# Kernel optimization log

Measured on AMD Instinct MI355X. Metric: run time of the kernel, lower is better.

## Reference

```python
import jax, jax.numpy as jnp
import numpy as np

N_HEAD = 16
HEAD_DIM = 64
ROPE_BASE = 10000.0


def _rope_tables(seq_len, head_dim):
    inv_freq = 1.0 / (ROPE_BASE ** (jnp.arange(0, head_dim, 2, dtype=jnp.float32) / head_dim))
    freqs = jnp.arange(seq_len, dtype=jnp.float32)[:, None] * inv_freq[None, :]  # (T, D/2)
    return jnp.cos(freqs), jnp.sin(freqs)


def _apply_rope(x, cos, sin):
    # x: (B, H, T, D); cos/sin: (T, D/2) broadcast to (1,1,T,D/2)
    x_even = x[..., ::2]
    x_odd = x[..., 1::2]
    re = x_even * cos - x_odd * sin
    ro = x_even * sin + x_odd * cos
    return jnp.stack((re, ro), axis=-1).reshape(x.shape)


def setup_inputs() -> dict:
    key = jax.random.key(0)
    ks = jax.random.split(key, 5)
    B, T, C = 4, 2048, 1024
    return {
        "x": jax.random.normal(ks[0], (B, T, C), dtype=jnp.float32),
        "qkv_w": jax.random.normal(ks[1], (3 * C, C), dtype=jnp.float32) * 0.02,
        "qkv_b": jax.random.normal(ks[2], (3 * C,), dtype=jnp.float32) * 0.02,
        "out_w": jax.random.normal(ks[3], (C, C), dtype=jnp.float32) * 0.02,
        "out_b": jax.random.normal(ks[4], (C,), dtype=jnp.float32) * 0.02,
    }


def reference(x, qkv_w, qkv_b, out_w, out_b):
    B, T, C = x.shape
    H, D = N_HEAD, HEAD_DIM
    qkv = x @ qkv_w.T + qkv_b                       # (B, T, 3C)
    qkv = qkv.reshape(B, T, 3, H, D).transpose(2, 0, 3, 1, 4)  # (3, B, H, T, D)
    q, k, v = qkv[0], qkv[1], qkv[2]
    cos, sin = _rope_tables(T, D)
    cos = cos[None, None]
    sin = sin[None, None]
    q = _apply_rope(q, cos, sin)
    k = _apply_rope(k, cos, sin)
    scores = jnp.einsum('bhtd,bhsd->bhts', q, k) / jnp.sqrt(jnp.float32(D))
    causal = jnp.tril(jnp.ones((T, T), dtype=bool))
    scores = jnp.where(causal[None, None], scores, -jnp.inf)
    weights = jax.nn.softmax(scores, axis=-1)
    out = jnp.einsum('bhts,bhsd->bhtd', weights, v)  # (B, H, T, D)
    out = out.transpose(0, 2, 1, 3).reshape(B, T, C)
    return out @ out_w.T + out_b
```

## Files before the change

kernel.cpp:

```cpp
#include <hip/hip_runtime.h>

#define B_ 4
#define T_ 2048
#define C_ 1024
#define H_ 16
#define D_ 64
#define M_ (B_*T_)
#define N1_ (3*C_)

typedef __bf16 bf16;
typedef __bf16 bf16x8 __attribute__((ext_vector_type(8)));
typedef __bf16 bf16x4 __attribute__((ext_vector_type(4)));
typedef float f32x4 __attribute__((ext_vector_type(4)));

#define GLOAD_LDS16(g, l) \
    __builtin_amdgcn_global_load_lds((const __attribute__((address_space(1))) void*)(g), \
                                     (__attribute__((address_space(3))) void*)(l), 16, 0, 0)

__global__ void k_conv3(const float* __restrict__ x, const float* __restrict__ w1,
                        const float* __restrict__ w2, bf16* __restrict__ xb,
                        bf16* __restrict__ wb1, bf16* __restrict__ wb2) {
    long i = ((long)blockIdx.x * 256 + threadIdx.x) * 4;
    const float* src; bf16* dst; long off;
    if (i < 8388608L)       { src = x;  dst = xb;  off = i; }
    else if (i < 11534336L) { src = w1; dst = wb1; off = i - 8388608L; }
    else                    { src = w2; dst = wb2; off = i - 11534336L; }
    float4 v = *(const float4*)(src + off);
    bf16x4 o; o[0] = (bf16)v.x; o[1] = (bf16)v.y; o[2] = (bf16)v.z; o[3] = (bf16)v.w;
    *(bf16x4*)(dst + off) = o;
}

__global__ __launch_bounds__(256) void k_gemm_qkv(const bf16* __restrict__ A,
                                                  const bf16* __restrict__ W,
                                                  const float* __restrict__ bias,
                                                  bf16* __restrict__ qr,
                                                  bf16* __restrict__ kr,
                                                  bf16* __restrict__ vt) {
    __shared__ __align__(16) bf16 As[128 * 32];
    __shared__ __align__(16) bf16 Ws[128 * 32];
    const int tid = threadIdx.x;
    const int lane16 = tid & 15;
    const int quad = (tid & 63) >> 4;
    const int wave = tid >> 6;
    const int wm = (wave >> 1) * 64, wn = (wave & 1) * 64;
    const long m0 = (long)blockIdx.y * 128;
    const long n0 = (long)blockIdx.x * 128;
    const int K = C_;

    f32x4 acc[4][4] = {};

    const int ra = tid >> 2, sa = tid & 3;
    const bf16* Ab0 = A + (m0 + ra) * K + sa * 8;
    const bf16* Ab1 = Ab0 + 64 * K;
    const bf16* Wb0 = W + (n0 + ra) * K + sa * 8;
    const bf16* Wb1 = Wb0 + 64 * K;
    bf16* Ad0 = As + tid * 8;
    bf16* Ad1 = As + tid * 8 + 2048;
    bf16* Wd0 = Ws + tid * 8;
    bf16* Wd1 = Ws + tid * 8 + 2048;

    for (int kt = 0; kt < K; kt += 32) {
        __syncthreads();
        GLOAD_LDS16(Ab0 + kt, Ad0);
        GLOAD_LDS16(Ab1 + kt, Ad1);
        GLOAD_LDS16(Wb0 + kt, Wd0);
        GLOAD_LDS16(Wb1 + kt, Wd1);
        __syncthreads();
        bf16x8 af[4], wf[4];
#pragma unroll
        for (int i = 0; i < 4; i++)
            af[i] = *(const bf16x8*)(As + (wm + i * 16 + lane16) * 32 + quad * 8);
#pragma unroll
        for (int i = 0; i < 4; i++)
            wf[i] = *(const bf16x8*)(Ws + (wn + i * 16 + lane16) * 32 + quad * 8);
#pragma unroll
        for (int mi = 0; mi < 4; mi++)
#pragma unroll
            for (int ni = 0; ni < 4; ni++)
                acc[mi][ni] = __builtin_amdgcn_mfma_f32_16x16x32_bf16(
                    af[mi], wf[ni], acc[mi][ni], 0, 0, 0);
    }

    const int sect = (int)blockIdx.x >> 3;
    const int bloc = (int)(m0 >> 11);
    const int tloc0 = ((int)m0 & 2047) + wm + quad * 4;

    if (sect < 2) {
        bf16* dst = (sect == 0) ? qr : kr;
#pragma unroll
        for (int ni = 0; ni < 4; ni++) {
            int n = (int)n0 + wn + ni * 16 + lane16;
            int d = n & 63;
            int h = (n >> 6) & 15;
            float bn = bias[n];
            float inv = exp2f(-0.415241011861f * (float)(d >> 1));
            float sb, cb; sincosf((float)tloc0 * inv, &sb, &cb);
            float s1, c1; sincosf(inv, &s1, &c1);
            float s16, c16; sincosf(16.0f * inv, &s16, &c16);
            bf16* base = dst + ((long)(bloc * 16 + h) * T_) * 64 + d;
#pragma unroll
            for (int mi = 0; mi < 4; mi++) {
                float cm = cb, sm = sb;
#pragma unroll
                for (int r = 0; r < 4; r++) {
                    float v = acc[mi][ni][r] + bn;
                    float vp = __shfl_xor(v, 1, 64);
                    float outv = (d & 1) ? (vp * sm + v * cm) : (v * cm - vp * sm);
                    base[(long)(tloc0 + mi * 16 + r) * 64] = (bf16)outv;
                    float cm2 = cm * c1 - sm * s1;
                    float sm2 = sm * c1 + cm * s1;
                    cm = cm2; sm = sm2;
                }
                float cb2 = cb * c16 - sb * s16;
                float sb2 = sb * c16 + cb * s16;
                cb = cb2; sb = sb2;
            }
        }
    } else {
#pragma unroll
        for (int ni = 0; ni < 4; ni++) {
            int n = (int)n0 + wn + ni * 16 + lane16;
            int d = n & 63;
            int h = (n >> 6) & 15;
            float bn = bias[n];
            bf16* base = vt + ((long)(bloc * 16 + h) * 64 + d) * T_ + tloc0;
#pragma unroll
            for (int mi = 0; mi < 4; mi++) {
                bf16x4 w;
#pragma unroll
                for (int r = 0; r < 4; r++) w[r] = (bf16)(acc[mi][ni][r] + bn);
                *(bf16x4*)(base + mi * 16) = w;
            }
        }
    }
}

__global__ __launch_bounds__(256) void k_gemm_out(const bf16* __restrict__ A,
                                                  const bf16* __restrict__ W,
                                                  const float* __restrict__ bias,
                                                  float* __restrict__ Cout) {
    __shared__ __align__(16) bf16 As[128 * 32];
    __shared__ __align__(16) bf16 Ws[128 * 32];
    const int tid = threadIdx.x;
    const int lane16 = tid & 15;
    const int quad = (tid & 63) >> 4;
    const int wave = tid >> 6;
    const int wm = (wave >> 1) * 64, wn = (wave & 1) * 64;
    const long m0 = (long)blockIdx.y * 128;
    const long n0 = (long)blockIdx.x * 128;
    const int K = C_, N = C_;

    f32x4 acc[4][4] = {};

    const int ra = tid >> 2, sa = tid & 3;
    const bf16* Ab0 = A + (m0 + ra) * K + sa * 8;
    const bf16* Ab1 = Ab0 + 64 * K;
    const bf16* Wb0 = W + (n0 + ra) * K + sa * 8;
    const bf16* Wb1 = Wb0 + 64 * K;
    bf16* Ad0 = As + tid * 8;
    bf16* Ad1 = As + tid * 8 + 2048;
    bf16* Wd0 = Ws + tid * 8;
    bf16* Wd1 = Ws + tid * 8 + 2048;

    for (int kt = 0; kt < K; kt += 32) {
        __syncthreads();
        GLOAD_LDS16(Ab0 + kt, Ad0);
        GLOAD_LDS16(Ab1 + kt, Ad1);
        GLOAD_LDS16(Wb0 + kt, Wd0);
        GLOAD_LDS16(Wb1 + kt, Wd1);
        __syncthreads();
        bf16x8 af[4], wf[4];
#pragma unroll
        for (int i = 0; i < 4; i++)
            af[i] = *(const bf16x8*)(As + (wm + i * 16 + lane16) * 32 + quad * 8);
#pragma unroll
        for (int i = 0; i < 4; i++)
            wf[i] = *(const bf16x8*)(Ws + (wn + i * 16 + lane16) * 32 + quad * 8);
#pragma unroll
        for (int mi = 0; mi < 4; mi++)
#pragma unroll
            for (int ni = 0; ni < 4; ni++)
                acc[mi][ni] = __builtin_amdgcn_mfma_f32_16x16x32_bf16(
                    af[mi], wf[ni], acc[mi][ni], 0, 0, 0);
    }

#pragma unroll
    for (int ni = 0; ni < 4; ni++) {
        long n = n0 + wn + ni * 16 + lane16;
        float bn = bias[n];
#pragma unroll
        for (int mi = 0; mi < 4; mi++) {
            long m = m0 + wm + mi * 16 + quad * 4;
#pragma unroll
            for (int r = 0; r < 4; r++)
                Cout[(m + r) * N + n] = acc[mi][ni][r] + bn;
        }
    }
}

__global__ __launch_bounds__(256) void k_flash(const bf16* __restrict__ qr,
                                               const bf16* __restrict__ kr,
                                               const bf16* __restrict__ vt,
                                               bf16* __restrict__ attn) {
    __shared__ __align__(16) bf16 Ks[64 * 72];
    __shared__ __align__(16) bf16 Vs[64 * 72];
    __shared__ __align__(16) bf16 Pl[8 * 16 * 72];

    const int bh = blockIdx.y;
    const int b = bh >> 4, h = bh & 15;
    const int tid = threadIdx.x;
    const int lane16 = tid & 15, quad = (tid & 63) >> 4;
    const int wave = tid >> 6;
    const int srow = tid >> 3, sch = tid & 7;

    const bf16* kbase = kr + (long)bh * T_ * 64;
    const bf16* vbase = vt + (long)bh * 64 * T_;
    bf16* Pw[2] = { Pl + (wave * 2 + 0) * (16 * 72), Pl + (wave * 2 + 1) * (16 * 72) };

    bf16x8 k0 = *(const bf16x8*)(kbase + (long)srow * 64 + sch * 8);
    bf16x8 k1 = *(const bf16x8*)(kbase + (long)(srow + 32) * 64 + sch * 8);
    bf16x8 v0 = *(const bf16x8*)(vbase + (long)srow * T_ + sch * 8);
    bf16x8 v1 = *(const bf16x8*)(vbase + (long)(srow + 32) * T_ + sch * 8);

    for (int phase = 0; phase < 2; ++phase) {
        const int qt = (phase == 0) ? (int)blockIdx.x : 15 - (int)blockIdx.x;
        const int qrow0[2] = { qt * 128 + wave * 16, qt * 128 + (wave + 4) * 16 };

        bf16x8 qf[2][2];
#pragma unroll
        for (int g = 0; g < 2; g++) {
            const bf16* qb = qr + ((long)bh * T_ + qrow0[g]) * 64 + lane16 * 64;
            qf[g][0] = *(const bf16x8*)(qb + quad * 8);
            qf[g][1] = *(const bf16x8*)(qb + 32 + quad * 8);
        }

        float m_i[2] = { -1e30f, -1e30f }, l_i[2] = { 0.f, 0.f };
        f32x4 o[2][4] = {};

        const int nkv = 2 * qt + 2;
        for (int kv = 0; kv < nkv; kv++) {
            const int s0 = kv * 64;
            __syncthreads();
            *(bf16x8*)(Ks + srow * 72 + sch * 8) = k0;
            *(bf16x8*)(Ks + (srow + 32) * 72 + sch * 8) = k1;
            *(bf16x8*)(Vs + srow * 72 + sch * 8) = v0;
            *(bf16x8*)(Vs + (srow + 32) * 72 + sch * 8) = v1;
            __syncthreads();

            {
                const int sn = (kv + 1 < nkv) ? (kv + 1) * 64 : 0;
                k0 = *(const bf16x8*)(kbase + (long)(sn + srow) * 64 + sch * 8);
                k1 = *(const bf16x8*)(kbase + (long)(sn + srow + 32) * 64 + sch * 8);
                v0 = *(const bf16x8*)(vbase + (long)srow * T_ + sn + sch * 8);
                v1 = *(const bf16x8*)(vbase + (long)(srow + 32) * T_ + sn + sch * 8);
            }

            f32x4 sacc[2][4];
#pragma unroll
            for (int ct = 0; ct < 4; ct++) {
                const bf16* krow = Ks + (ct * 16 + lane16) * 72;
                bf16x8 kf0 = *(const bf16x8*)(krow + quad * 8);
                bf16x8 kf1 = *(const bf16x8*)(krow + 32 + quad * 8);
                f32x4 z0 = {}, z1 = {};
                z0 = __builtin_amdgcn_mfma_f32_16x16x32_bf16(kf0, qf[0][0], z0, 0, 0, 0);
                sacc[0][ct] = __builtin_amdgcn_mfma_f32_16x16x32_bf16(kf1, qf[0][1], z0, 0, 0, 0);
                z1 = __builtin_amdgcn_mfma_f32_16x16x32_bf16(kf0, qf[1][0], z1, 0, 0, 0);
                sacc[1][ct] = __builtin_amdgcn_mfma_f32_16x16x32_bf16(kf1, qf[1][1], z1, 0, 0, 0);
            }

            float p[2][4][4];
#pragma unroll
            for (int g = 0; g < 2; g++) {
                if (s0 + 63 > qrow0[g]) {
                    const int qg = qrow0[g] + lane16;
#pragma unroll
                    for (int ct = 0; ct < 4; ct++)
#pragma unroll
                        for (int r = 0; r < 4; r++) {
                            int sg = s0 + ct * 16 + quad * 4 + r;
                            p[g][ct][r] = (sg > qg) ? -1e30f : sacc[g][ct][r] * 0.125f;
                        }
                } else {
#pragma unroll
                    for (int ct = 0; ct < 4; ct++)
#pragma unroll
                        for (int r = 0; r < 4; r++)
                            p[g][ct][r] = sacc[g][ct][r] * 0.125f;
                }
                float tm = p[g][0][0];
#pragma unroll
                for (int ct = 0; ct < 4; ct++)
#pragma unroll
                    for (int r = 0; r < 4; r++) tm = fmaxf(tm, p[g][ct][r]);
                tm = fmaxf(tm, __shfl_xor(tm, 16, 64));
                tm = fmaxf(tm, __shfl_xor(tm, 32, 64));
                float mn = fmaxf(m_i[g], tm);
                float alpha = __expf(m_i[g] - mn);
                m_i[g] = mn;
                float ps = 0.f;
#pragma unroll
                for (int ct = 0; ct < 4; ct++)
#pragma unroll
                    for (int r = 0; r < 4; r++) {
                        p[g][ct][r] = __expf(p[g][ct][r] - mn);
                        ps += p[g][ct][r];
                    }
                ps += __shfl_xor(ps, 16, 64);
                ps += __shfl_xor(ps, 32, 64);
                l_i[g] = l_i[g] * alpha + ps;
#pragma unroll
                for (int dt = 0; dt < 4; dt++)
#pragma unroll
                    for (int r = 0; r < 4; r++) o[g][dt][r] *= alpha;
            }

#pragma unroll
            for (int g = 0; g < 2; g++)
#pragma unroll
                for (int ct = 0; ct < 4; ct++) {
                    bf16x4 w;
                    w[0] = (bf16)p[g][ct][0]; w[1] = (bf16)p[g][ct][1];
                    w[2] = (bf16)p[g][ct][2]; w[3] = (bf16)p[g][ct][3];
                    *(bf16x4*)(Pw[g] + lane16 * 72 + ct * 16 + quad * 4) = w;
                }
            __builtin_amdgcn_wave_barrier();
            bf16x8 pf[2][2];
#pragma unroll
            for (int g = 0; g < 2; g++) {
                pf[g][0] = *(const bf16x8*)(Pw[g] + lane16 * 72 + quad * 8);
                pf[g][1] = *(const bf16x8*)(Pw[g] + lane16 * 72 + 32 + quad * 8);
            }

#pragma unroll
            for (int dt = 0; dt < 4; dt++) {
                const bf16* vrow = Vs + (dt * 16 + lane16) * 72;
                bf16x8 vf0 = *(const bf16x8*)(vrow + quad * 8);
                bf16x8 vf1 = *(const bf16x8*)(vrow + 32 + quad * 8);
                o[0][dt] = __builtin_amdgcn_mfma_f32_16x16x32_bf16(vf0, pf[0][0], o[0][dt], 0, 0, 0);
                o[0][dt] = __builtin_amdgcn_mfma_f32_16x16x32_bf16(vf1, pf[0][1], o[0][dt], 0, 0, 0);
                o[1][dt] = __builtin_amdgcn_mfma_f32_16x16x32_bf16(vf0, pf[1][0], o[1][dt], 0, 0, 0);
                o[1][dt] = __builtin_amdgcn_mfma_f32_16x16x32_bf16(vf1, pf[1][1], o[1][dt], 0, 0, 0);
            }
        }

#pragma unroll
        for (int g = 0; g < 2; g++) {
            float invl = 1.0f / l_i[g];
            bf16* orow = attn + ((long)b * T_ + qrow0[g] + lane16) * C_ + h * 64 + quad * 4;
#pragma unroll
            for (int dt = 0; dt < 4; dt++) {
                bf16x4 w;
                w[0] = (bf16)(o[g][dt][0] * invl); w[1] = (bf16)(o[g][dt][1] * invl);
                w[2] = (bf16)(o[g][dt][2] * invl); w[3] = (bf16)(o[g][dt][3] * invl);
                *(bf16x4*)(orow + dt * 16) = w;
            }
        }
    }
}

extern "C" void kernel_launch(void* const* d_in, const int* in_sizes, int n_in,
                              void* d_out, int out_size, void* d_ws, size_t ws_size,
                              hipStream_t stream) {
    const float* x     = (const float*)d_in[0];
    const float* qkv_w = (const float*)d_in[1];
    const float* qkv_b = (const float*)d_in[2];
    const float* out_w = (const float*)d_in[3];
    const float* out_b = (const float*)d_in[4];
    char* ws = (char*)d_ws;

    bf16* xb   = (bf16*)(ws + 0);
    bf16* wqkv = (bf16*)(ws + 16777216);
    bf16* wout = (bf16*)(ws + 23068672);
    bf16* qr   = (bf16*)(ws + 25165824);
    bf16* kr   = (bf16*)(ws + 41943040);
    bf16* vt   = (bf16*)(ws + 58720256);
    bf16* attn = (bf16*)(ws + 75497472);

    k_conv3<<<12288, 256, 0, stream>>>(x, qkv_w, out_w, xb, wqkv, wout);

    k_gemm_qkv<<<dim3(24, 64), 256, 0, stream>>>(xb, wqkv, qkv_b, qr, kr, vt);

    k_flash<<<dim3(8, 64), 256, 0, stream>>>(qr, kr, vt, attn);

    k_gemm_out<<<dim3(8, 64), 256, 0, stream>>>(attn, wout, out_b, (float*)d_out);
}
```

Baseline: 280.0 us.

## Widen GEMM K-tile with swizzled LDS, fold softmax scale into Q, split flash phases

Both GEMMs now stage a 64-wide K slice per iteration into LDS using an XOR swizzle, halving the number of barrier pairs and reducing LDS bank conflicts. The softmax scale and log2(e) factor are folded into Q during the QKV epilogue, so the flash kernel uses exp2f and skips the per-score multiply. The flash kernel no longer pairs two query tiles per block; it launches one block per query tile (16 per head), ordered longest-first, which doubles the grid and gives up the paired-tile load balancing.

```diff
diff --git a/kernel.cpp b/kernel.cpp
--- a/kernel.cpp
+++ b/kernel.cpp
@@ -7,6 +7,7 @@
 #define D_ 64
 #define M_ (B_*T_)
 #define N1_ (3*C_)
+#define QSCALE 0.18033688011112042f
 
 typedef __bf16 bf16;
 typedef __bf16 bf16x8 __attribute__((ext_vector_type(8)));
@@ -30,14 +31,49 @@
     *(bf16x4*)(dst + off) = o;
 }
 
+#define GEMM_KLOOP(A, W, K)                                                          \
+    const int ra = tid >> 3, sa = tid & 7;                                           \
+    const int cl = sa ^ (ra & 7);                                                    \
+    const bf16* Ab = (A) + (m0 + ra) * (K) + cl * 8;                                 \
+    const bf16* Wb = (W) + (n0 + ra) * (K) + cl * 8;                                 \
+    bf16* Ad = As + tid * 8;                                                         \
+    bf16* Wd = Ws + tid * 8;                                                         \
+    const int sq = quad ^ (lane16 & 7);                                              \
+    for (int kt = 0; kt < (K); kt += 64) {                                           \
+        __syncthreads();                                                             \
+        _Pragma("unroll")                                                            \
+        for (int j = 0; j < 4; j++) {                                                \
+            GLOAD_LDS16(Ab + (long)(32 * j) * (K) + kt, Ad + j * 2048);              \
+            GLOAD_LDS16(Wb + (long)(32 * j) * (K) + kt, Wd + j * 2048);              \
+        }                                                                            \
+        __syncthreads();                                                             \
+        _Pragma("unroll")                                                            \
+        for (int kk = 0; kk < 2; kk++) {                                             \
+            bf16x8 af[4], wf[4];                                                     \
+            const int so = ((kk * 4) ^ sq) * 8;      \
+            _Pragma("unroll")                                                        \
+            for (int i = 0; i < 4; i++)                                              \
+                af[i] = *(const bf16x8*)(As + (wm + i * 16 + lane16) * 64 + (so ^ (kk * 4 * 8 * 0)));\
+            _Pragma("unroll")                                                        \
+            for (int i = 0; i < 4; i++)                                              \
+                wf[i] = *(const bf16x8*)(Ws + (wn + i * 16 + lane16) * 64 + so);     \
+            _Pragma("unroll")                                                        \
+            for (int mi = 0; mi < 4; mi++)                                           \
+                _Pragma("unroll")                                                    \
+                for (int ni = 0; ni < 4; ni++)                                       \
+                    acc[mi][ni] = __builtin_amdgcn_mfma_f32_16x16x32_bf16(           \
+                        af[mi], wf[ni], acc[mi][ni], 0, 0, 0);                       \
+        }                                                                            \
+    }
+
 __global__ __launch_bounds__(256) void k_gemm_qkv(const bf16* __restrict__ A,
                                                   const bf16* __restrict__ W,
                                                   const float* __restrict__ bias,
                                                   bf16* __restrict__ qr,
                                                   bf16* __restrict__ kr,
                                                   bf16* __restrict__ vt) {
-    __shared__ __align__(16) bf16 As[128 * 32];
-    __shared__ __align__(16) bf16 Ws[128 * 32];
+    __shared__ __align__(16) bf16 As[128 * 64];
+    __shared__ __align__(16) bf16 Ws[128 * 64];
     const int tid = threadIdx.x;
     const int lane16 = tid & 15;
     const int quad = (tid & 63) >> 4;
@@ -45,41 +81,9 @@
     const int wm = (wave >> 1) * 64, wn = (wave & 1) * 64;
     const long m0 = (long)blockIdx.y * 128;
     const long n0 = (long)blockIdx.x * 128;
-    const int K = C_;
 
     f32x4 acc[4][4] = {};
-
-    const int ra = tid >> 2, sa = tid & 3;
-    const bf16* Ab0 = A + (m0 + ra) * K + sa * 8;
-    const bf16* Ab1 = Ab0 + 64 * K;
-    const bf16* Wb0 = W + (n0 + ra) * K + sa * 8;
-    const bf16* Wb1 = Wb0 + 64 * K;
-    bf16* Ad0 = As + tid * 8;
-    bf16* Ad1 = As + tid * 8 + 2048;
-    bf16* Wd0 = Ws + tid * 8;
-    bf16* Wd1 = Ws + tid * 8 + 2048;
-
-    for (int kt = 0; kt < K; kt += 32) {
-        __syncthreads();
-        GLOAD_LDS16(Ab0 + kt, Ad0);
-        GLOAD_LDS16(Ab1 + kt, Ad1);
-        GLOAD_LDS16(Wb0 + kt, Wd0);
-        GLOAD_LDS16(Wb1 + kt, Wd1);
-        __syncthreads();
-        bf16x8 af[4], wf[4];
-#pragma unroll
-        for (int i = 0; i < 4; i++)
-            af[i] = *(const bf16x8*)(As + (wm + i * 16 + lane16) * 32 + quad * 8);
-#pragma unroll
-        for (int i = 0; i < 4; i++)
-            wf[i] = *(const bf16x8*)(Ws + (wn + i * 16 + lane16) * 32 + quad * 8);
-#pragma unroll
-        for (int mi = 0; mi < 4; mi++)
-#pragma unroll
-            for (int ni = 0; ni < 4; ni++)
-                acc[mi][ni] = __builtin_amdgcn_mfma_f32_16x16x32_bf16(
-                    af[mi], wf[ni], acc[mi][ni], 0, 0, 0);
-    }
+    GEMM_KLOOP(A, W, C_)
 
     const int sect = (int)blockIdx.x >> 3;
     const int bloc = (int)(m0 >> 11);
@@ -87,6 +91,7 @@
 
     if (sect < 2) {
         bf16* dst = (sect == 0) ? qr : kr;
+        const float osc = (sect == 0) ? QSCALE : 1.0f;
 #pragma unroll
         for (int ni = 0; ni < 4; ni++) {
             int n = (int)n0 + wn + ni * 16 + lane16;
@@ -106,7 +111,7 @@
                     float v = acc[mi][ni][r] + bn;
                     float vp = __shfl_xor(v, 1, 64);
                     float outv = (d & 1) ? (vp * sm + v * cm) : (v * cm - vp * sm);
-                    base[(long)(tloc0 + mi * 16 + r) * 64] = (bf16)outv;
+                    base[(long)(tloc0 + mi * 16 + r) * 64] = (bf16)(outv * osc);
                     float cm2 = cm * c1 - sm * s1;
                     float sm2 = sm * c1 + cm * s1;
                     cm = cm2; sm = sm2;
@@ -139,8 +144,8 @@
                                                   const bf16* __restrict__ W,
                                                   const float* __restrict__ bias,
                                                   float* __restrict__ Cout) {
-    __shared__ __align__(16) bf16 As[128 * 32];
-    __shared__ __align__(16) bf16 Ws[128 * 32];
+    __shared__ __align__(16) bf16 As[128 * 64];
+    __shared__ __align__(16) bf16 Ws[128 * 64];
     const int tid = threadIdx.x;
     const int lane16 = tid & 15;
     const int quad = (tid & 63) >> 4;
@@ -148,41 +153,10 @@
     const int wm = (wave >> 1) * 64, wn = (wave & 1) * 64;
     const long m0 = (long)blockIdx.y * 128;
     const long n0 = (long)blockIdx.x * 128;
-    const int K = C_, N = C_;
+    const int N = C_;
 
     f32x4 acc[4][4] = {};
-
-    const int ra = tid >> 2, sa = tid & 3;
-    const bf16* Ab0 = A + (m0 + ra) * K + sa * 8;
-    const bf16* Ab1 = Ab0 + 64 * K;
-    const bf16* Wb0 = W + (n0 + ra) * K + sa * 8;
-    const bf16* Wb1 = Wb0 + 64 * K;
-    bf16* Ad0 = As + tid * 8;
-    bf16* Ad1 = As + tid * 8 + 2048;
-    bf16* Wd0 = Ws + tid * 8;
-    bf16* Wd1 = Ws + tid * 8 + 2048;
-
-    for (int kt = 0; kt < K; kt += 32) {
-        __syncthreads();
-        GLOAD_LDS16(Ab0 + kt, Ad0);
-        GLOAD_LDS16(Ab1 + kt, Ad1);
-        GLOAD_LDS16(Wb0 + kt, Wd0);
-        GLOAD_LDS16(Wb1 + kt, Wd1);
-        __syncthreads();
-        bf16x8 af[4], wf[4];
-#pragma unroll
-        for (int i = 0; i < 4; i++)
-            af[i] = *(const bf16x8*)(As + (wm + i * 16 + lane16) * 32 + quad * 8);
-#pragma unroll
-        for (int i = 0; i < 4; i++)
-            wf[i] = *(const bf16x8*)(Ws + (wn + i * 16 + lane16) * 32 + quad * 8);
-#pragma unroll
-        for (int mi = 0; mi < 4; mi++)
-#pragma unroll
-            for (int ni = 0; ni < 4; ni++)
-                acc[mi][ni] = __builtin_amdgcn_mfma_f32_16x16x32_bf16(
-                    af[mi], wf[ni], acc[mi][ni], 0, 0, 0);
-    }
+    GEMM_KLOOP(A, W, C_)
 
 #pragma unroll
     for (int ni = 0; ni < 4; ni++) {
@@ -217,143 +191,141 @@
     const bf16* vbase = vt + (long)bh * 64 * T_;
     bf16* Pw[2] = { Pl + (wave * 2 + 0) * (16 * 72), Pl + (wave * 2 + 1) * (16 * 72) };
 
+    const int qt = 15 - (int)blockIdx.x;
+    const int qrow0[2] = { qt * 128 + wave * 16, qt * 128 + (wave + 4) * 16 };
+
     bf16x8 k0 = *(const bf16x8*)(kbase + (long)srow * 64 + sch * 8);
     bf16x8 k1 = *(const bf16x8*)(kbase + (long)(srow + 32) * 64 + sch * 8);
     bf16x8 v0 = *(const bf16x8*)(vbase + (long)srow * T_ + sch * 8);
     bf16x8 v1 = *(const bf16x8*)(vbase + (long)(srow + 32) * T_ + sch * 8);
 
-    for (int phase = 0; phase < 2; ++phase) {
-        const int qt = (phase == 0) ? (int)blockIdx.x : 15 - (int)blockIdx.x;
-        const int qrow0[2] = { qt * 128 + wave * 16, qt * 128 + (wave + 4) * 16 };
-
-        bf16x8 qf[2][2];
+    bf16x8 qf[2][2];
+#pragma unroll
+    for (int g = 0; g < 2; g++) {
+        const bf16* qb = qr + ((long)bh * T_ + qrow0[g]) * 64 + lane16 * 64;
+        qf[g][0] = *(const bf16x8*)(qb + quad * 8);
+        qf[g][1] = *(const bf16x8*)(qb + 32 + quad * 8);
+    }
+
+    float m_i[2] = { -1e30f, -1e30f }, l_i[2] = { 0.f, 0.f };
+    f32x4 o[2][4] = {};
+
+    const int nkv = 2 * qt + 2;
+    for (int kv = 0; kv < nkv; kv++) {
+        const int s0 = kv * 64;
+        __syncthreads();
+        *(bf16x8*)(Ks + srow * 72 + sch * 8) = k0;
+        *(bf16x8*)(Ks + (srow + 32) * 72 + sch * 8) = k1;
+        *(bf16x8*)(Vs + srow * 72 + sch * 8) = v0;
+        *(bf16x8*)(Vs + (srow + 32) * 72 + sch * 8) = v1;
+        __syncthreads();
+
+        {
+            const int sn = (kv + 1 < nkv) ? (kv + 1) * 64 : 0;
+            k0 = *(const bf16x8*)(kbase + (long)(sn + srow) * 64 + sch * 8);
+            k1 = *(const bf16x8*)(kbase + (long)(sn + srow + 32) * 64 + sch * 8);
+            v0 = *(const bf16x8*)(vbase + (long)srow * T_ + sn + sch * 8);
+            v1 = *(const bf16x8*)(vbase + (long)(srow + 32) * T_ + sn + sch * 8);
+        }
+
+        f32x4 sacc[2][4];
+#pragma unroll
+        for (int ct = 0; ct < 4; ct++) {
+            const bf16* krow = Ks + (ct * 16 + lane16) * 72;
+            bf16x8 kf0 = *(const bf16x8*)(krow + quad * 8);
+            bf16x8 kf1 = *(const bf16x8*)(krow + 32 + quad * 8);
+            f32x4 z0 = {}, z1 = {};
+            z0 = __builtin_amdgcn_mfma_f32_16x16x32_bf16(kf0, qf[0][0], z0, 0, 0, 0);
+            sacc[0][ct] = __builtin_amdgcn_mfma_f32_16x16x32_bf16(kf1, qf[0][1], z0, 0, 0, 0);
+            z1 = __builtin_amdgcn_mfma_f32_16x16x32_bf16(kf0, qf[1][0], z1, 0, 0, 0);
+            sacc[1][ct] = __builtin_amdgcn_mfma_f32_16x16x32_bf16(kf1, qf[1][1], z1, 0, 0, 0);
+        }
+
+        float p[2][4][4];
 #pragma unroll
         for (int g = 0; g < 2; g++) {
-            const bf16* qb = qr + ((long)bh * T_ + qrow0[g]) * 64 + lane16 * 64;
-            qf[g][0] = *(const bf16x8*)(qb + quad * 8);
-            qf[g][1] = *(const bf16x8*)(qb + 32 + quad * 8);
-        }
-
-        float m_i[2] = { -1e30f, -1e30f }, l_i[2] = { 0.f, 0.f };
-        f32x4 o[2][4] = {};
-
-        const int nkv = 2 * qt + 2;
-        for (int kv = 0; kv < nkv; kv++) {
-            const int s0 = kv * 64;
-            __syncthreads();
-            *(bf16x8*)(Ks + srow * 72 + sch * 8) = k0;
-            *(bf16x8*)(Ks + (srow + 32) * 72 + sch * 8) = k1;
-            *(bf16x8*)(Vs + srow * 72 + sch * 8) = v0;
-            *(bf16x8*)(Vs + (srow + 32) * 72 + sch * 8) = v1;
-            __syncthreads();
-
-            {
-                const int sn = (kv + 1 < nkv) ? (kv + 1) * 64 : 0;
-                k0 = *(const bf16x8*)(kbase + (long)(sn + srow) * 64 + sch * 8);
-                k1 = *(const bf16x8*)(kbase + (long)(sn + srow + 32) * 64 + sch * 8);
-                v0 = *(const bf16x8*)(vbase + (long)srow * T_ + sn + sch * 8);
-                v1 = *(const bf16x8*)(vbase + (long)(srow + 32) * T_ + sn + sch * 8);
+            if (s0 + 63 > qrow0[g]) {
+                const int qg = qrow0[g] + lane16;
+#pragma unroll
+                for (int ct = 0; ct < 4; ct++)
+#pragma unroll
+                    for (int r = 0; r < 4; r++) {
+                        int sg = s0 + ct * 16 + quad * 4 + r;
+                        p[g][ct][r] = (sg > qg) ? -1e30f : sacc[g][ct][r];
+                    }
+            } else {
+#pragma unroll
+                for (int ct = 0; ct < 4; ct++)
+#pragma unroll
+                    for (int r = 0; r < 4; r++)
+                        p[g][ct][r] = sacc[g][ct][r];
             }
-
-            f32x4 sacc[2][4];
+            float tm = p[g][0][0];
+#pragma unroll
+            for (int ct = 0; ct < 4; ct++)
+#pragma unroll
+                for (int r = 0; r < 4; r++) tm = fmaxf(tm, p[g][ct][r]);
+            tm = fmaxf(tm, __shfl_xor(tm, 16, 64));
+            tm = fmaxf(tm, __shfl_xor(tm, 32, 64));
+            float mn = fmaxf(m_i[g], tm);
+            float alpha = exp2f(m_i[g] - mn);
+            m_i[g] = mn;
+            float ps = 0.f;
+#pragma unroll
+            for (int ct = 0; ct < 4; ct++)
+#pragma unroll
+                for (int r = 0; r < 4; r++) {
+                    p[g][ct][r] = exp2f(p[g][ct][r] - mn);
+                    ps += p[g][ct][r];
+                }
+            ps += __shfl_xor(ps, 16, 64);
+            ps += __shfl_xor(ps, 32, 64);
+            l_i[g] = l_i[g] * alpha + ps;
+#pragma unroll
+            for (int dt = 0; dt < 4; dt++)
+#pragma unroll
+                for (int r = 0; r < 4; r++) o[g][dt][r] *= alpha;
+        }
+
+#pragma unroll
+        for (int g = 0; g < 2; g++)
 #pragma unroll
             for (int ct = 0; ct < 4; ct++) {
-                const bf16* krow = Ks + (ct * 16 + lane16) * 72;
-                bf16x8 kf0 = *(const bf16x8*)(krow + quad * 8);
-                bf16x8 kf1 = *(const bf16x8*)(krow + 32 + quad * 8);
-                f32x4 z0 = {}, z1 = {};
-                z0 = __builtin_amdgcn_mfma_f32_16x16x32_bf16(kf0, qf[0][0], z0, 0, 0, 0);
-                sacc[0][ct] = __builtin_amdgcn_mfma_f32_16x16x32_bf16(kf1, qf[0][1], z0, 0, 0, 0);
-                z1 = __builtin_amdgcn_mfma_f32_16x16x32_bf16(kf0, qf[1][0], z1, 0, 0, 0);
-                sacc[1][ct] = __builtin_amdgcn_mfma_f32_16x16x32_bf16(kf1, qf[1][1], z1, 0, 0, 0);
+                bf16x4 w;
+                w[0] = (bf16)p[g][ct][0]; w[1] = (bf16)p[g][ct][1];
+                w[2] = (bf16)p[g][ct][2]; w[3] = (bf16)p[g][ct][3];
+                *(bf16x4*)(Pw[g] + lane16 * 72 + ct * 16 + quad * 4) = w;
             }
-
-            float p[2][4][4];
-#pragma unroll
-            for (int g = 0; g < 2; g++) {
-                if (s0 + 63 > qrow0[g]) {
-                    const int qg = qrow0[g] + lane16;
-#pragma unroll
-                    for (int ct = 0; ct < 4; ct++)
-#pragma unroll
-                        for (int r = 0; r < 4; r++) {
-                            int sg = s0 + ct * 16 + quad * 4 + r;
-                            p[g][ct][r] = (sg > qg) ? -1e30f : sacc[g][ct][r] * 0.125f;
-                        }
-                } else {
-#pragma unroll
-                    for (int ct = 0; ct < 4; ct++)
-#pragma unroll
-                        for (int r = 0; r < 4; r++)
-                            p[g][ct][r] = sacc[g][ct][r] * 0.125f;
-                }
-                float tm = p[g][0][0];
-#pragma unroll
-                for (int ct = 0; ct < 4; ct++)
-#pragma unroll
-                    for (int r = 0; r < 4; r++) tm = fmaxf(tm, p[g][ct][r]);
-                tm = fmaxf(tm, __shfl_xor(tm, 16, 64));
-                tm = fmaxf(tm, __shfl_xor(tm, 32, 64));
-                float mn = fmaxf(m_i[g], tm);
-                float alpha = __expf(m_i[g] - mn);
-                m_i[g] = mn;
-                float ps = 0.f;
-#pragma unroll
-                for (int ct = 0; ct < 4; ct++)
-#pragma unroll
-                    for (int r = 0; r < 4; r++) {
-                        p[g][ct][r] = __expf(p[g][ct][r] - mn);
-                        ps += p[g][ct][r];
-                    }
-                ps += __shfl_xor(ps, 16, 64);
-                ps += __shfl_xor(ps, 32, 64);
-                l_i[g] = l_i[g] * alpha + ps;
-#pragma unroll
-                for (int dt = 0; dt < 4; dt++)
-#pragma unroll
-                    for (int r = 0; r < 4; r++) o[g][dt][r] *= alpha;
-            }
-
-#pragma unroll
-            for (int g = 0; g < 2; g++)
-#pragma unroll
-                for (int ct = 0; ct < 4; ct++) {
-                    bf16x4 w;
-                    w[0] = (bf16)p[g][ct][0]; w[1] = (bf16)p[g][ct][1];
-                    w[2] = (bf16)p[g][ct][2]; w[3] = (bf16)p[g][ct][3];
-                    *(bf16x4*)(Pw[g] + lane16 * 72 + ct * 16 + quad * 4) = w;
-                }
-            __builtin_amdgcn_wave_barrier();
-            bf16x8 pf[2][2];
-#pragma unroll
-            for (int g = 0; g < 2; g++) {
-                pf[g][0] = *(const bf16x8*)(Pw[g] + lane16 * 72 + quad * 8);
-                pf[g][1] = *(const bf16x8*)(Pw[g] + lane16 * 72 + 32 + quad * 8);
-            }
-
-#pragma unroll
-            for (int dt = 0; dt < 4; dt++) {
-                const bf16* vrow = Vs + (dt * 16 + lane16) * 72;
-                bf16x8 vf0 = *(const bf16x8*)(vrow + quad * 8);
-                bf16x8 vf1 = *(const bf16x8*)(vrow + 32 + quad * 8);
-                o[0][dt] = __builtin_amdgcn_mfma_f32_16x16x32_bf16(vf0, pf[0][0], o[0][dt], 0, 0, 0);
-                o[0][dt] = __builtin_amdgcn_mfma_f32_16x16x32_bf16(vf1, pf[0][1], o[0][dt], 0, 0, 0);
-                o[1][dt] = __builtin_amdgcn_mfma_f32_16x16x32_bf16(vf0, pf[1][0], o[1][dt], 0, 0, 0);
-                o[1][dt] = __builtin_amdgcn_mfma_f32_16x16x32_bf16(vf1, pf[1][1], o[1][dt], 0, 0, 0);
-            }
-        }
-
+        __builtin_amdgcn_wave_barrier();
+        bf16x8 pf[2][2];
 #pragma unroll
         for (int g = 0; g < 2; g++) {
-            float invl = 1.0f / l_i[g];
-            bf16* orow = attn + ((long)b * T_ + qrow0[g] + lane16) * C_ + h * 64 + quad * 4;
-#pragma unroll
-            for (int dt = 0; dt < 4; dt++) {
-                bf16x4 w;
-                w[0] = (bf16)(o[g][dt][0] * invl); w[1] = (bf16)(o[g][dt][1] * invl);
-                w[2] = (bf16)(o[g][dt][2] * invl); w[3] = (bf16)(o[g][dt][3] * invl);
-                *(bf16x4*)(orow + dt * 16) = w;
-            }
+            pf[g][0] = *(const bf16x8*)(Pw[g] + lane16 * 72 + quad * 8);
+            pf[g][1] = *(const bf16x8*)(Pw[g] + lane16 * 72 + 32 + quad * 8);
+        }
+
+#pragma unroll
+        for (int dt = 0; dt < 4; dt++) {
+            const bf16* vrow = Vs + (dt * 16 + lane16) * 72;
+            bf16x8 vf0 = *(const bf16x8*)(vrow + quad * 8);
+            bf16x8 vf1 = *(const bf16x8*)(vrow + 32 + quad * 8);
+            o[0][dt] = __builtin_amdgcn_mfma_f32_16x16x32_bf16(vf0, pf[0][0], o[0][dt], 0, 0, 0);
+            o[0][dt] = __builtin_amdgcn_mfma_f32_16x16x32_bf16(vf1, pf[0][1], o[0][dt], 0, 0, 0);
+            o[1][dt] = __builtin_amdgcn_mfma_f32_16x16x32_bf16(vf0, pf[1][0], o[1][dt], 0, 0, 0);
+            o[1][dt] = __builtin_amdgcn_mfma_f32_16x16x32_bf16(vf1, pf[1][1], o[1][dt], 0, 0, 0);
+        }
+    }
+
+#pragma unroll
+    for (int g = 0; g < 2; g++) {
+        float invl = 1.0f / l_i[g];
+        bf16* orow = attn + ((long)b * T_ + qrow0[g] + lane16) * C_ + h * 64 + quad * 4;
+#pragma unroll
+        for (int dt = 0; dt < 4; dt++) {
+            bf16x4 w;
+            w[0] = (bf16)(o[g][dt][0] * invl); w[1] = (bf16)(o[g][dt][1] * invl);
+            w[2] = (bf16)(o[g][dt][2] * invl); w[3] = (bf16)(o[g][dt][3] * invl);
+            *(bf16x4*)(orow + dt * 16) = w;
         }
     }
 }
@@ -380,7 +352,7 @@
 
     k_gemm_qkv<<<dim3(24, 64), 256, 0, stream>>>(xb, wqkv, qkv_b, qr, kr, vt);
 
-    k_flash<<<dim3(8, 64), 256, 0, stream>>>(qr, kr, vt, attn);
+    k_flash<<<dim3(16, 64), 256, 0, stream>>>(qr, kr, vt, attn);
 
     k_gemm_out<<<dim3(8, 64), 256, 0, stream>>>(attn, wout, out_b, (float*)d_out);
 }
```

Result: slower. 350.1 us (+25.0%).
